# Kernel tuning notes

Hardware: AMD Instinct MI355X
Metric: run time of the kernel (lower is better)

Reference implementation:

```python
import jax, jax.numpy as jnp
import numpy as np
from jax import lax

KERNEL = 31
SMOOTH = 0.001
PAD = KERNEL // 2


def _avg_pool2d(x):
    # torch F.avg_pool2d(kernel=31, stride=1, padding=15, count_include_pad=True):
    # sum over 31x31 window with zero padding, then divide by 31*31 always.
    s = lax.reduce_window(
        x, 0.0, lax.add,
        window_dimensions=(1, 1, KERNEL, KERNEL),
        window_strides=(1, 1, 1, 1),
        padding=((0, 0), (0, 0), (PAD, PAD), (PAD, PAD)),
    )
    return s / (KERNEL * KERNEL)


def setup_inputs() -> dict:
    key = jax.random.key(0)
    k1, k2 = jax.random.split(key)
    B, C, H, W = 32, 1, 1024, 1024
    output = jax.random.normal(k1, (B, C, H, W), dtype=jnp.float32)
    target = jax.random.uniform(k2, (B, C, H, W), dtype=jnp.float32)
    return {"output": output, "target": target}


def reference(output, target):
    out = jax.nn.sigmoid(output)
    weight = 1.0 + 5.0 * jnp.abs(_avg_pool2d(target) - target)  # [B,C,H,W]
    inter = jnp.sum(out * target * weight, axis=(2, 3)).reshape(-1, 1)      # [B*C,1]
    mask_sum = jnp.sum((target + out) * weight, axis=(2, 3)).reshape(-1, 1)  # [B*C,1]
    loss = 1.0 - (2.0 * inter + SMOOTH) / (mask_sum + SMOOTH)
    return jnp.mean(loss)
```

## Files before the change

### kernel.cpp

```cpp
#include <hip/hip_runtime.h>
#include <math.h>


namespace {
constexpr int Bn = 32;
constexpr int Hn = 1024;
constexpr int Wn = 1024;
constexpr int Rn = 15;
constexpr int TX = 256;
constexpr int YS = 64;
constexpr int NB = YS / 8;
constexpr int NCOL = TX + 32;
constexpr int PHYSW = (NCOL / 8) * 12;
constexpr float INV_KK = 1.0f / 961.0f;
}

__device__ __forceinline__ int phys(int i) { return i + ((i >> 3) << 2); }

__device__ __forceinline__ float ldcol(const float* p, int y, int col, bool xok) {
    return (xok && (unsigned)y < (unsigned)Hn) ? p[(size_t)y * Wn + col] : 0.0f;
}

__global__ __launch_bounds__(256, 6)
void dice_main(const float* __restrict__ logits, const float* __restrict__ tgt,
               float* __restrict__ acc)
{
    __shared__ __align__(16) float vbuf[8 * PHYSW];
    __shared__ float red[8];

    const int bid = blockIdx.x;
    const int b   = bid >> 6;
    const int rem = bid & 63;
    const int x0  = (rem >> 4) * TX;
    const int y0  = (rem & 15) * YS;
    const int t   = threadIdx.x;

    const float* tb = tgt    + (size_t)b * Hn * Wn;
    const float* ob = logits + (size_t)b * Hn * Wn;

    const int  col0 = x0 - Rn + t;
    const bool has2 = (t < 32);
    const int  col1 = col0 + 256;
    const bool xok0 = (col0 >= 0);
    const bool xok1 = (col1 < Wn);
    const int  pt   = phys(t);
    const int  pt2  = phys(256 + t);

    const int r0 = t >> 6;
    const int jj = t & 63;
    const int xb = x0 + (jj << 2);

    float vs0 = 0.0f, vs1 = 0.0f;
    for (int yy = y0 - Rn; yy <= y0 + Rn; ++yy) {
        vs0 += ldcol(tb, yy, col0, xok0);
        if (has2) vs1 += ldcol(tb, yy, col1, xok1);
    }

    float acc_i = 0.0f, acc_m = 0.0f;

    for (int it = 0; it < NB; ++it) {
        const int ya = y0 + it * 8;

        #pragma unroll
        for (int r = 0; r < 8; ++r) {
            const int yr = ya + r;
            if (it > 0 || r > 0) {
                vs0 += ldcol(tb, yr + Rn, col0, xok0) - ldcol(tb, yr - Rn - 1, col0, xok0);
                if (has2) vs1 += ldcol(tb, yr + Rn, col1, xok1) - ldcol(tb, yr - Rn - 1, col1, xok1);
            }
            vbuf[r * PHYSW + pt] = vs0;
            if (has2) vbuf[r * PHYSW + pt2] = vs1;
        }
        __syncthreads();

        #pragma unroll
        for (int ss = 0; ss < 2; ++ss) {
            const int  row  = r0 + ss * 4;
            const int  yrow = ya + row;
            const float* vr = &vbuf[row * PHYSW];
            const int  base = jj << 2;

            const float4 tc4 = *(const float4*)(tb + (size_t)yrow * Wn + xb);
            const float4 oc4 = *(const float4*)(ob + (size_t)yrow * Wn + xb);

            const float4 a = *(const float4*)&vr[phys(base)];
            float s = a.w;
            #pragma unroll
            for (int k = 1; k < 7; ++k) {
                const float4 q = *(const float4*)&vr[phys(base + 4 * k)];
                s += (q.x + q.y) + (q.z + q.w);
            }
            const float4 h = *(const float4*)&vr[phys(base + 28)];
            s += (h.x + h.y) + h.z;
            const float4 g = *(const float4*)&vr[phys(base + 32)];

            float sm = s + (a.x + a.y) + a.z;
            const float tcv[4]  = {tc4.x, tc4.y, tc4.z, tc4.w};
            const float ocv[4]  = {oc4.x, oc4.y, oc4.z, oc4.w};
            const float wsub[3] = {a.x, a.y, a.z};
            const float wadd[3] = {h.w, g.x, g.y};

            #pragma unroll
            for (int m = 0; m < 4; ++m) {
                if (m > 0) sm += wadd[m - 1] - wsub[m - 1];
                const float avg = sm * INV_KK;
                const float wt  = 1.0f + 5.0f * fabsf(avg - tcv[m]);
                const float sg  = 1.0f / (1.0f + __expf(-ocv[m]));
                acc_i += sg * tcv[m] * wt;
                acc_m += (tcv[m] + sg) * wt;
            }
        }
        __syncthreads();
    }

    #pragma unroll
    for (int off = 32; off > 0; off >>= 1) {
        acc_i += __shfl_down(acc_i, off);
        acc_m += __shfl_down(acc_m, off);
    }
    const int lane = t & 63;
    const int wv   = t >> 6;
    if (lane == 0) { red[wv * 2] = acc_i; red[wv * 2 + 1] = acc_m; }
    __syncthreads();
    if (t == 0) {
        atomicAdd(&acc[2 * b],     red[0] + red[2] + red[4] + red[6]);
        atomicAdd(&acc[2 * b + 1], red[1] + red[3] + red[5] + red[7]);
    }
}

__global__ void dice_final(const float* __restrict__ acc, float* __restrict__ out)
{
    const int t = threadIdx.x;
    float l = 0.0f;
    if (t < Bn) {
        const float I = acc[2 * t];
        const float M = acc[2 * t + 1];
        l = 1.0f - (2.0f * I + 0.001f) / (M + 0.001f);
    }
    #pragma unroll
    for (int off = 32; off > 0; off >>= 1) l += __shfl_down(l, off);
    if (t == 0) out[0] = l * (1.0f / 32.0f);
}

extern "C" void kernel_launch(void* const* d_in, const int* in_sizes, int n_in,
                              void* d_out, int out_size, void* d_ws, size_t ws_size,
                              hipStream_t stream)
{
    const float* logits = (const float*)d_in[0];
    const float* target = (const float*)d_in[1];
    float* acc = (float*)d_ws;

    hipMemsetAsync(d_ws, 0, 64 * sizeof(float), stream);
    dice_main<<<dim3(Bn * 64), dim3(256), 0, stream>>>(logits, target, acc);
    dice_final<<<dim3(1), dim3(64), 0, stream>>>(acc, (float*)d_out);
}
```

Before: 361.6 us.

## Give each wavefront its own tile and drop block-wide barriers

Each 64-lane wavefront now owns a full 256x64 tile. It keeps five column sums in registers, has a private shared-memory row buffer, and processes one row per iteration, so there is no __syncthreads. Loads for the next row and for the sliding-window add and subtract are software-prefetched one iteration ahead. The intent is to remove the block barriers and overlap memory latency. In exchange, register pressure rises and the launch bound drops from 6 to 2 blocks per CU, while the grid shrinks by a factor of four, which may reduce parallelism.

```diff
diff --git a/kernel.cpp b/kernel.cpp
--- a/kernel.cpp
+++ b/kernel.cpp
@@ -7,110 +7,150 @@
 constexpr int Hn = 1024;
 constexpr int Wn = 1024;
 constexpr int Rn = 15;
-constexpr int TX = 256;
-constexpr int YS = 64;
-constexpr int NB = YS / 8;
-constexpr int NCOL = TX + 32;
+constexpr int XS = 256;
+constexpr int YSW = 64;
+constexpr int NCOL = XS + 32;
 constexpr int PHYSW = (NCOL / 8) * 12;
+constexpr int WPB = 4;
 constexpr float INV_KK = 1.0f / 961.0f;
 }
 
 __device__ __forceinline__ int phys(int i) { return i + ((i >> 3) << 2); }
 
-__device__ __forceinline__ float ldcol(const float* p, int y, int col, bool xok) {
-    return (xok && (unsigned)y < (unsigned)Hn) ? p[(size_t)y * Wn + col] : 0.0f;
+__device__ __forceinline__ float ldc(const float* rowp, int c, bool ok) {
+    return ok ? rowp[c] : 0.0f;
 }
 
-__global__ __launch_bounds__(256, 6)
+__global__ __launch_bounds__(256, 2)
 void dice_main(const float* __restrict__ logits, const float* __restrict__ tgt,
                float* __restrict__ acc)
 {
-    __shared__ __align__(16) float vbuf[8 * PHYSW];
-    __shared__ float red[8];
+    __shared__ __align__(16) float vbuf[WPB][PHYSW];
 
-    const int bid = blockIdx.x;
-    const int b   = bid >> 6;
-    const int rem = bid & 63;
-    const int x0  = (rem >> 4) * TX;
-    const int y0  = (rem & 15) * YS;
-    const int t   = threadIdx.x;
+    const int t   = threadIdx.x & 63;
+    const int wid = threadIdx.x >> 6;
+    const int gw  = blockIdx.x * WPB + wid;
+
+    const int b   = gw >> 6;
+    const int rem = gw & 63;
+    const int x0  = (rem >> 4) * XS;
+    const int y0  = (rem & 15) * YSW;
 
     const float* tb = tgt    + (size_t)b * Hn * Wn;
     const float* ob = logits + (size_t)b * Hn * Wn;
+    float* wb = vbuf[wid];
 
-    const int  col0 = x0 - Rn + t;
-    const bool has2 = (t < 32);
-    const int  col1 = col0 + 256;
-    const bool xok0 = (col0 >= 0);
-    const bool xok1 = (col1 < Wn);
-    const int  pt   = phys(t);
-    const int  pt2  = phys(256 + t);
+    const int  c0   = x0 - Rn + t;
+    const bool hasv4 = (t < 32);
+    const int  c4   = x0 - Rn + 256 + t;
+    const bool xok0 = (c0 >= 0);
+    const bool xok4 = (c4 < Wn);
 
-    const int r0 = t >> 6;
-    const int jj = t & 63;
-    const int xb = x0 + (jj << 2);
+    const int xb   = x0 + (t << 2);
+    const int base = t << 2;
 
-    float vs0 = 0.0f, vs1 = 0.0f;
+    float vs0 = 0.f, vs1 = 0.f, vs2 = 0.f, vs3 = 0.f, vs4 = 0.f;
     for (int yy = y0 - Rn; yy <= y0 + Rn; ++yy) {
-        vs0 += ldcol(tb, yy, col0, xok0);
-        if (has2) vs1 += ldcol(tb, yy, col1, xok1);
+        if ((unsigned)yy < (unsigned)Hn) {
+            const float* rp = tb + (size_t)yy * Wn;
+            vs0 += ldc(rp, c0, xok0);
+            vs1 += rp[c0 + 64];
+            vs2 += rp[c0 + 128];
+            vs3 += rp[c0 + 192];
+            if (hasv4) vs4 += ldc(rp, c4, xok4);
+        }
     }
 
-    float acc_i = 0.0f, acc_m = 0.0f;
+    float4 ct = *(const float4*)(tb + (size_t)y0 * Wn + xb);
+    float4 co = *(const float4*)(ob + (size_t)y0 * Wn + xb);
 
-    for (int it = 0; it < NB; ++it) {
-        const int ya = y0 + it * 8;
+    float na0 = 0.f, na1 = 0.f, na2 = 0.f, na3 = 0.f, na4 = 0.f;
+    float nu0 = 0.f, nu1 = 0.f, nu2 = 0.f, nu3 = 0.f, nu4 = 0.f;
+    {
+        const int ya = y0 + 1 + Rn, yu = y0 - Rn;
+        if ((unsigned)ya < (unsigned)Hn) {
+            const float* rp = tb + (size_t)ya * Wn;
+            na0 = ldc(rp, c0, xok0); na1 = rp[c0 + 64];
+            na2 = rp[c0 + 128];      na3 = rp[c0 + 192];
+            if (hasv4) na4 = ldc(rp, c4, xok4);
+        }
+        if ((unsigned)yu < (unsigned)Hn) {
+            const float* rp = tb + (size_t)yu * Wn;
+            nu0 = ldc(rp, c0, xok0); nu1 = rp[c0 + 64];
+            nu2 = rp[c0 + 128];      nu3 = rp[c0 + 192];
+            if (hasv4) nu4 = ldc(rp, c4, xok4);
+        }
+    }
 
-        #pragma unroll
-        for (int r = 0; r < 8; ++r) {
-            const int yr = ya + r;
-            if (it > 0 || r > 0) {
-                vs0 += ldcol(tb, yr + Rn, col0, xok0) - ldcol(tb, yr - Rn - 1, col0, xok0);
-                if (has2) vs1 += ldcol(tb, yr + Rn, col1, xok1) - ldcol(tb, yr - Rn - 1, col1, xok1);
-            }
-            vbuf[r * PHYSW + pt] = vs0;
-            if (has2) vbuf[r * PHYSW + pt2] = vs1;
+    float acc_i = 0.f, acc_m = 0.f;
+
+    #pragma unroll 2
+    for (int r = 0; r < YSW; ++r) {
+        const int y = y0 + r;
+
+        wb[phys(t)]        = vs0;
+        wb[phys(64 + t)]   = vs1;
+        wb[phys(128 + t)]  = vs2;
+        wb[phys(192 + t)]  = vs3;
+        if (hasv4) wb[phys(256 + t)] = vs4;
+
+        float4 nt, no;
+        if (r + 1 < YSW) {
+            nt = *(const float4*)(tb + (size_t)(y + 1) * Wn + xb);
+            no = *(const float4*)(ob + (size_t)(y + 1) * Wn + xb);
         }
-        __syncthreads();
 
-        #pragma unroll
-        for (int ss = 0; ss < 2; ++ss) {
-            const int  row  = r0 + ss * 4;
-            const int  yrow = ya + row;
-            const float* vr = &vbuf[row * PHYSW];
-            const int  base = jj << 2;
-
-            const float4 tc4 = *(const float4*)(tb + (size_t)yrow * Wn + xb);
-            const float4 oc4 = *(const float4*)(ob + (size_t)yrow * Wn + xb);
-
-            const float4 a = *(const float4*)&vr[phys(base)];
-            float s = a.w;
+        {
+            const float4 A  = *(const float4*)&wb[phys(base)];
+            float mid = 0.f;
             #pragma unroll
             for (int k = 1; k < 7; ++k) {
-                const float4 q = *(const float4*)&vr[phys(base + 4 * k)];
-                s += (q.x + q.y) + (q.z + q.w);
+                const float4 q = *(const float4*)&wb[phys(base + (k << 2))];
+                mid += (q.x + q.y) + (q.z + q.w);
             }
-            const float4 h = *(const float4*)&vr[phys(base + 28)];
-            s += (h.x + h.y) + h.z;
-            const float4 g = *(const float4*)&vr[phys(base + 32)];
+            const float4 Hh = *(const float4*)&wb[phys(base + 28)];
+            const float4 G  = *(const float4*)&wb[phys(base + 32)];
 
-            float sm = s + (a.x + a.y) + a.z;
-            const float tcv[4]  = {tc4.x, tc4.y, tc4.z, tc4.w};
-            const float ocv[4]  = {oc4.x, oc4.y, oc4.z, oc4.w};
-            const float wsub[3] = {a.x, a.y, a.z};
-            const float wadd[3] = {h.w, g.x, g.y};
+            float wsum = mid + (A.x + A.y) + (A.z + A.w)
+                             + (Hh.x + Hh.y) + Hh.z;
+            const float tcv[4]  = {ct.x, ct.y, ct.z, ct.w};
+            const float ocv[4]  = {co.x, co.y, co.z, co.w};
+            const float wsub[3] = {A.x, A.y, A.z};
+            const float wadd[3] = {Hh.w, G.x, G.y};
 
             #pragma unroll
             for (int m = 0; m < 4; ++m) {
-                if (m > 0) sm += wadd[m - 1] - wsub[m - 1];
-                const float avg = sm * INV_KK;
+                if (m > 0) wsum += wadd[m - 1] - wsub[m - 1];
+                const float avg = wsum * INV_KK;
                 const float wt  = 1.0f + 5.0f * fabsf(avg - tcv[m]);
                 const float sg  = 1.0f / (1.0f + __expf(-ocv[m]));
                 acc_i += sg * tcv[m] * wt;
                 acc_m += (tcv[m] + sg) * wt;
             }
         }
-        __syncthreads();
+
+        if (r + 1 < YSW) {
+            vs0 += na0 - nu0; vs1 += na1 - nu1; vs2 += na2 - nu2;
+            vs3 += na3 - nu3;
+            if (hasv4) vs4 += na4 - nu4;
+            ct = nt; co = no;
+
+            if (r + 2 < YSW) {
+                const int ya = y + 2 + Rn, yu = y + 2 - Rn - 1;
+                if ((unsigned)ya < (unsigned)Hn) {
+                    const float* rp = tb + (size_t)ya * Wn;
+                    na0 = ldc(rp, c0, xok0); na1 = rp[c0 + 64];
+                    na2 = rp[c0 + 128];      na3 = rp[c0 + 192];
+                    if (hasv4) na4 = ldc(rp, c4, xok4);
+                } else { na0 = na1 = na2 = na3 = na4 = 0.f; }
+                if ((unsigned)yu < (unsigned)Hn) {
+                    const float* rp = tb + (size_t)yu * Wn;
+                    nu0 = ldc(rp, c0, xok0); nu1 = rp[c0 + 64];
+                    nu2 = rp[c0 + 128];      nu3 = rp[c0 + 192];
+                    if (hasv4) nu4 = ldc(rp, c4, xok4);
+                } else { nu0 = nu1 = nu2 = nu3 = nu4 = 0.f; }
+            }
+        }
     }
 
     #pragma unroll
@@ -118,13 +158,9 @@
         acc_i += __shfl_down(acc_i, off);
         acc_m += __shfl_down(acc_m, off);
     }
-    const int lane = t & 63;
-    const int wv   = t >> 6;
-    if (lane == 0) { red[wv * 2] = acc_i; red[wv * 2 + 1] = acc_m; }
-    __syncthreads();
     if (t == 0) {
-        atomicAdd(&acc[2 * b],     red[0] + red[2] + red[4] + red[6]);
-        atomicAdd(&acc[2 * b + 1], red[1] + red[3] + red[5] + red[7]);
+        atomicAdd(&acc[2 * b],     acc_i);
+        atomicAdd(&acc[2 * b + 1], acc_m);
     }
 }
 
@@ -151,6 +187,6 @@
     float* acc = (float*)d_ws;
 
     hipMemsetAsync(d_ws, 0, 64 * sizeof(float), stream);
-    dice_main<<<dim3(Bn * 64), dim3(256), 0, stream>>>(logits, target, acc);
+    dice_main<<<dim3(Bn * 64 / WPB), dim3(256), 0, stream>>>(logits, target, acc);
     dice_final<<<dim3(1), dim3(64), 0, stream>>>(acc, (float*)d_out);
 }
```

New measurement: 319.0 us. 11.8% less time.
